# Optimization experiments

Measured on AMD Instinct MI355X. Metric: run time of the kernel, lower is better.

The kernel has to match this reference:

```python
import jax, jax.numpy as jnp
import numpy as np

N_NODES, IN_F, HIDDEN, N_EDGES, N_TRAIN, N_CLASS = 50000, 64, 512, 160000, 80000, 7
BN_EPS = 1e-5

def _lin(k, fin, fout):
    return jax.random.normal(k, (fin, fout), jnp.float32) * 0.05, jnp.zeros((fout,), jnp.float32)

def setup_inputs() -> dict:
    key = jax.random.key(0)
    ks = jax.random.split(key, 12)
    x = jax.random.normal(ks[0], (N_NODES, IN_F), jnp.float32)
    edge_index = jax.random.randint(ks[1], (2, N_EDGES), 0, N_NODES, jnp.int32)
    train_edge_id = jax.random.randint(ks[2], (N_TRAIN,), 0, N_EDGES, jnp.int32)
    W1, b1 = _lin(ks[3], IN_F, HIDDEN)
    W2, b2 = _lin(ks[4], HIDDEN, HIDDEN)
    W3, b3 = _lin(ks[5], HIDDEN, HIDDEN)
    W4, b4 = _lin(ks[6], HIDDEN, HIDDEN)
    lin1_W, lin1_b = _lin(ks[7], HIDDEN, HIDDEN)
    lin2_W, lin2_b = _lin(ks[8], HIDDEN, HIDDEN)
    fc2_W, fc2_b = _lin(ks[9], HIDDEN, N_CLASS)
    ones = jnp.ones((HIDDEN,), jnp.float32); zeros = jnp.zeros((HIDDEN,), jnp.float32)
    return dict(x=x, edge_index=edge_index, train_edge_id=train_edge_id,
                W1=W1, b1=b1, W2=W2, b2=b2, W3=W3, b3=b3,
                bn1_g=ones, bn1_b=zeros, bn1_m=zeros, bn1_v=ones, eps1=jnp.float32(0.0),
                W4=W4, b4=b4, bn2_g=ones, bn2_b=zeros, bn2_m=zeros, bn2_v=ones, eps2=jnp.float32(0.0),
                lin1_W=lin1_W, lin1_b=lin1_b, lin2_W=lin2_W, lin2_b=lin2_b,
                fc2_W=fc2_W, fc2_b=fc2_b)

def _gin_agg(h, src, dst, eps):
    # PyG GINConv: (1+eps)*x_i + sum_{j in N(i)} x_j, messages flow src->dst
    agg = jax.ops.segment_sum(h[src], dst, num_segments=N_NODES)
    return (1.0 + eps) * h + agg

def _bn(h, g, b, m, v):
    return (h - m) * jax.lax.rsqrt(v + BN_EPS) * g + b

def reference(x, edge_index, train_edge_id, W1, b1, W2, b2, W3, b3,
              bn1_g, bn1_b, bn1_m, bn1_v, eps1,
              W4, b4, bn2_g, bn2_b, bn2_m, bn2_v, eps2,
              lin1_W, lin1_b, lin2_W, lin2_b, fc2_W, fc2_b):
    src, dst = edge_index[0], edge_index[1]
    h = _gin_agg(x, src, dst, eps1)
    h = jax.nn.relu(h @ W1 + b1)
    h = jax.nn.relu(h @ W2 + b2)
    h = jax.nn.relu(h @ W3 + b3)
    h = _bn(h, bn1_g, bn1_b, bn1_m, bn1_v)
    # gin_convs[0]: agg -> Linear+ReLU -> BN
    h = _gin_agg(h, src, dst, eps2)
    h = jax.nn.relu(h @ W4 + b4)
    h = _bn(h, bn2_g, bn2_b, bn2_m, bn2_v)
    # node MLP head (dropout = identity in eval)
    h = jax.nn.relu(h @ lin1_W + lin1_b)
    h = h @ lin2_W + lin2_b
    # edge-gather fusion (feature_fusion=None -> elementwise mul)
    node_id = edge_index[:, train_edge_id]  # [2, T]
    x1 = h[node_id[0]]
    x2 = h[node_id[1]]
    return (x1 * x2) @ fc2_W + fc2_b  # [T, class_num]
```

## Files before the change

kernel.cpp:

```cpp
#include <hip/hip_runtime.h>

#define N_NODES 50000
#define MPAD    50048
#define IN_F    64
#define HIDDEN  512
#define N_EDGES 160000
#define N_TRAIN 80000
#define N_CLASS 7
#define BN_EPS  1e-5f

#define MT      (MPAD / 128)
#define NT      4
#define FULLGRP ((MT / 8) * 32)

typedef short  bf16x8 __attribute__((ext_vector_type(8)));
typedef float  f32x4  __attribute__((ext_vector_type(4)));
typedef unsigned short ushort_t;

__device__ __forceinline__ ushort_t f2b(float v) {
    union { float f; unsigned int u; } c; c.f = v;
    unsigned int x = c.u;
    unsigned int r = (x + 0x7FFFu + ((x >> 16) & 1u)) >> 16;
    return (ushort_t)r;
}
__device__ __forceinline__ float b2f(ushort_t b) {
    union { unsigned int u; float f; } c; c.u = ((unsigned int)b) << 16;
    return c.f;
}

__device__ __forceinline__ void async_copy16(const void* g, void* l) {
    __builtin_amdgcn_global_load_lds(
        (const __attribute__((address_space(1))) void*)g,
        (__attribute__((address_space(3))) void*)l, 16, 0, 0);
}

__global__ void zero_kernel(int* __restrict__ p, int n) {
    int i = blockIdx.x * blockDim.x + threadIdx.x;
    if (i < n) p[i] = 0;
}

__global__ void hist_kernel(const int* __restrict__ ei, int* __restrict__ deg) {
    int e = blockIdx.x * blockDim.x + threadIdx.x;
    if (e >= N_EDGES) return;
    atomicAdd(&deg[ei[N_EDGES + e]], 1);
}

__global__ __launch_bounds__(1024) void scan_kernel(const int* __restrict__ deg,
                                                    int* __restrict__ rowptr) {
    __shared__ int buf[1024];
    __shared__ int carry_s;
    int tid = threadIdx.x;
    if (tid == 0) { carry_s = 0; rowptr[0] = 0; }
    __syncthreads();
    for (int base = 0; base < N_NODES; base += 1024) {
        int i = base + tid;
        buf[tid] = (i < N_NODES) ? deg[i] : 0;
        __syncthreads();
        for (int off = 1; off < 1024; off <<= 1) {
            int t = (tid >= off) ? buf[tid - off] : 0;
            __syncthreads();
            buf[tid] += t;
            __syncthreads();
        }
        if (i < N_NODES) rowptr[i + 1] = buf[tid] + carry_s;
        __syncthreads();
        if (tid == 0) carry_s += buf[1023];
        __syncthreads();
    }
}

__global__ void cursor_init_kernel(const int* __restrict__ rowptr,
                                   int* __restrict__ cursor) {
    int i = blockIdx.x * blockDim.x + threadIdx.x;
    if (i < N_NODES) cursor[i] = rowptr[i];
}

__global__ void scatter_kernel(const int* __restrict__ ei,
                               int* __restrict__ cursor, int* __restrict__ adj) {
    int e = blockIdx.x * blockDim.x + threadIdx.x;
    if (e >= N_EDGES) return;
    int src = ei[e], dst = ei[N_EDGES + e];
    int pos = atomicAdd(&cursor[dst], 1);
    adj[pos] = src;
}

__global__ __launch_bounds__(256) void gather64_kernel(
    const float* __restrict__ x, const int* __restrict__ rowptr,
    const int* __restrict__ adj, const float* __restrict__ epsp,
    ushort_t* __restrict__ hi, ushort_t* __restrict__ lo) {
    int wave = threadIdx.x >> 6, lane = threadIdx.x & 63;
    int n = blockIdx.x * 4 + wave;
    if (n >= N_NODES) return;
    float s = 1.0f + *epsp;
    float sum = s * x[(size_t)n * IN_F + lane];
    int beg = rowptr[n], end = rowptr[n + 1];
    for (int k = beg; k < end; k++) {
        sum += x[(size_t)adj[k] * IN_F + lane];
    }
    ushort_t hb = f2b(sum);
    ushort_t lb = f2b(sum - b2f(hb));
    hi[(size_t)n * IN_F + lane] = hb;
    lo[(size_t)n * IN_F + lane] = lb;
}

__global__ __launch_bounds__(256) void gather512_kernel(
    const float* __restrict__ h, const int* __restrict__ rowptr,
    const int* __restrict__ adj, const float* __restrict__ epsp,
    ushort_t* __restrict__ hi, ushort_t* __restrict__ lo) {
    int wave = threadIdx.x >> 6, lane = threadIdx.x & 63;
    int n = blockIdx.x * 4 + wave;
    if (n >= N_NODES) return;
    float s = 1.0f + *epsp;
    const float* hn = h + (size_t)n * HIDDEN;
    const int f0 = lane * 4, f1 = 256 + lane * 4;
    float4 a0 = *(const float4*)&hn[f0];
    float4 a1 = *(const float4*)&hn[f1];
    float sum0[4] = {s * a0.x, s * a0.y, s * a0.z, s * a0.w};
    float sum1[4] = {s * a1.x, s * a1.y, s * a1.z, s * a1.w};
    int beg = rowptr[n], end = rowptr[n + 1];
    for (int k = beg; k < end; k++) {
        const float* hs = h + (size_t)adj[k] * HIDDEN;
        float4 b0 = *(const float4*)&hs[f0];
        float4 b1 = *(const float4*)&hs[f1];
        sum0[0] += b0.x; sum0[1] += b0.y; sum0[2] += b0.z; sum0[3] += b0.w;
        sum1[0] += b1.x; sum1[1] += b1.y; sum1[2] += b1.z; sum1[3] += b1.w;
    }
    ushort_t h4[4], l4[4];
#pragma unroll
    for (int j = 0; j < 4; j++) {
        h4[j] = f2b(sum0[j]);
        l4[j] = f2b(sum0[j] - b2f(h4[j]));
    }
    *(ushort4*)&hi[(size_t)n * HIDDEN + f0] = make_ushort4(h4[0], h4[1], h4[2], h4[3]);
    *(ushort4*)&lo[(size_t)n * HIDDEN + f0] = make_ushort4(l4[0], l4[1], l4[2], l4[3]);
#pragma unroll
    for (int j = 0; j < 4; j++) {
        h4[j] = f2b(sum1[j]);
        l4[j] = f2b(sum1[j] - b2f(h4[j]));
    }
    *(ushort4*)&hi[(size_t)n * HIDDEN + f1] = make_ushort4(h4[0], h4[1], h4[2], h4[3]);
    *(ushort4*)&lo[(size_t)n * HIDDEN + f1] = make_ushort4(l4[0], l4[1], l4[2], l4[3]);
}

__global__ void wtrans_kernel(const float* __restrict__ W,
                              ushort_t* __restrict__ Whi,
                              ushort_t* __restrict__ Wlo, int K) {
    __shared__ float t[32][33];
    int tx = threadIdx.x & 31, ty = threadIdx.x >> 5;
    int nb = blockIdx.x * 32, kb = blockIdx.y * 32;
#pragma unroll
    for (int i = 0; i < 4; i++) {
        int k = kb + ty + i * 8;
        t[ty + i * 8][tx] = W[(size_t)k * HIDDEN + nb + tx];
    }
    __syncthreads();
#pragma unroll
    for (int i = 0; i < 4; i++) {
        int n = nb + ty + i * 8;
        int k = kb + tx;
        float v = t[tx][ty + i * 8];
        ushort_t hb = f2b(v);
        ushort_t lb = f2b(v - b2f(hb));
        Whi[(size_t)n * K + k] = hb;
        Wlo[(size_t)n * K + k] = lb;
    }
}

__global__ __launch_bounds__(256) void gemm_split_kernel(
    const ushort_t* __restrict__ Ahi, const ushort_t* __restrict__ Alo,
    const ushort_t* __restrict__ Bhi, const ushort_t* __restrict__ Blo,
    const float* __restrict__ bias,
    float* __restrict__ Cf, ushort_t* __restrict__ Chi, ushort_t* __restrict__ Clo,
    int K, int mode,
    const float* __restrict__ bn_g, const float* __restrict__ bn_b,
    const float* __restrict__ bn_m, const float* __restrict__ bn_v) {
    __shared__ ushort_t As_h[128 * 32];
    __shared__ ushort_t As_l[128 * 32];
    __shared__ ushort_t Bs_h[128 * 32];
    __shared__ ushort_t Bs_l[128 * 32];

    const int tid  = threadIdx.x;
    const int wave = tid >> 6, lane = tid & 63;
    const int wm = wave >> 1, wn = wave & 1;
    const int quad = lane >> 4, r = lane & 15;

    int idx = blockIdx.x, m_t, n_t;
    if (idx < FULLGRP) {
        m_t = (idx >> 5) * 8 + (idx & 7);
        n_t = (idx >> 3) & 3;
    } else {
        int t = idx - FULLGRP;
        m_t = (FULLGRP >> 2) + (t >> 2);
        n_t = t & 3;
    }
    const int m0 = m_t * 128, n0 = n_t * 128;

    const f32x4 vzero = {0.f, 0.f, 0.f, 0.f};
    f32x4 acc[4][4];
#pragma unroll
    for (int i = 0; i < 4; i++)
#pragma unroll
        for (int j = 0; j < 4; j++) acc[i][j] = vzero;

    const int srow = (lane >> 2);
    const int scol = (lane & 3) * 8;

    for (int k0 = 0; k0 < K; k0 += 32) {
        __syncthreads();
#pragma unroll
        for (int t = 0; t < 2; t++) {
            int rr = wave * 32 + t * 16 + srow;
            int lbase = (wave * 32 + t * 16) * 32;
            size_t ga = (size_t)(m0 + rr) * K + k0 + scol;
            size_t gb = (size_t)(n0 + rr) * K + k0 + scol;
            async_copy16(Ahi + ga, &As_h[lbase]);
            async_copy16(Alo + ga, &As_l[lbase]);
            async_copy16(Bhi + gb, &Bs_h[lbase]);
            async_copy16(Blo + gb, &Bs_l[lbase]);
        }
        __syncthreads();

        bf16x8 ah[4], al[4], bh[4], bl[4];
#pragma unroll
        for (int i = 0; i < 4; i++) {
            int aofs = (wm * 64 + i * 16 + r) * 32 + quad * 8;
            int bofs = (wn * 64 + i * 16 + r) * 32 + quad * 8;
            ah[i] = *(const bf16x8*)&As_h[aofs];
            al[i] = *(const bf16x8*)&As_l[aofs];
            bh[i] = *(const bf16x8*)&Bs_h[bofs];
            bl[i] = *(const bf16x8*)&Bs_l[bofs];
        }
#pragma unroll
        for (int i = 0; i < 4; i++)
#pragma unroll
            for (int j = 0; j < 4; j++) {
                acc[i][j] = __builtin_amdgcn_mfma_f32_16x16x32_bf16(ah[i], bh[j], acc[i][j], 0, 0, 0);
                acc[i][j] = __builtin_amdgcn_mfma_f32_16x16x32_bf16(ah[i], bl[j], acc[i][j], 0, 0, 0);
                acc[i][j] = __builtin_amdgcn_mfma_f32_16x16x32_bf16(al[i], bh[j], acc[i][j], 0, 0, 0);
            }
    }

    float bia[4], sc[4], sh[4];
#pragma unroll
    for (int j = 0; j < 4; j++) {
        int col = n0 + wn * 64 + j * 16 + r;
        bia[j] = bias[col];
        if (mode == 2) {
            float g = bn_g[col], bb = bn_b[col], mm = bn_m[col], vv = bn_v[col];
            sc[j] = g * rsqrtf(vv + BN_EPS);
            sh[j] = bb - mm * sc[j];
        } else { sc[j] = 1.f; sh[j] = 0.f; }
    }
#pragma unroll
    for (int i = 0; i < 4; i++) {
#pragma unroll
        for (int rg = 0; rg < 4; rg++) {
            int row = m0 + wm * 64 + i * 16 + quad * 4 + rg;
            if (row >= N_NODES) continue;
#pragma unroll
            for (int j = 0; j < 4; j++) {
                int col = n0 + wn * 64 + j * 16 + r;
                float v = acc[i][j][rg] + bia[j];
                if (mode >= 1) v = fmaxf(v, 0.f);
                if (mode == 2) v = v * sc[j] + sh[j];
                size_t idx2 = (size_t)row * HIDDEN + col;
                if (Cf) {
                    Cf[idx2] = v;
                } else {
                    ushort_t hb = f2b(v);
                    ushort_t lb = f2b(v - b2f(hb));
                    Chi[idx2] = hb;
                    Clo[idx2] = lb;
                }
            }
        }
    }
}

__global__ __launch_bounds__(256) void fc2_kernel(
    const float* __restrict__ h, const int* __restrict__ ei,
    const int* __restrict__ teid, const float* __restrict__ W,
    const float* __restrict__ bias, float* __restrict__ out) {
    __shared__ float Ws[HIDDEN * N_CLASS];
    __shared__ float bs[N_CLASS];
    for (int i = threadIdx.x; i < HIDDEN * N_CLASS; i += blockDim.x) Ws[i] = W[i];
    if (threadIdx.x < N_CLASS) bs[threadIdx.x] = bias[threadIdx.x];
    __syncthreads();

    int wave = threadIdx.x >> 6;
    int lane = threadIdx.x & 63;
    int t = blockIdx.x * 4 + wave;
    if (t >= N_TRAIN) return;

    int e = teid[t];
    int a = ei[e];
    int b = ei[N_EDGES + e];
    const float* xa = h + (size_t)a * HIDDEN;
    const float* xb = h + (size_t)b * HIDDEN;

    float acc[N_CLASS];
#pragma unroll
    for (int c = 0; c < N_CLASS; c++) acc[c] = 0.f;

    int j0 = lane * 8;
    float4 a0 = *(const float4*)&xa[j0];
    float4 a1 = *(const float4*)&xa[j0 + 4];
    float4 b0 = *(const float4*)&xb[j0];
    float4 b1 = *(const float4*)&xb[j0 + 4];
    float p[8] = {a0.x * b0.x, a0.y * b0.y, a0.z * b0.z, a0.w * b0.w,
                  a1.x * b1.x, a1.y * b1.y, a1.z * b1.z, a1.w * b1.w};
#pragma unroll
    for (int jj = 0; jj < 8; jj++) {
        const float* wrow = &Ws[(j0 + jj) * N_CLASS];
#pragma unroll
        for (int c = 0; c < N_CLASS; c++) acc[c] = fmaf(p[jj], wrow[c], acc[c]);
    }
#pragma unroll
    for (int c = 0; c < N_CLASS; c++) {
        float v = acc[c];
        for (int off = 32; off > 0; off >>= 1) v += __shfl_down(v, off, 64);
        if (lane == 0) out[(size_t)t * N_CLASS + c] = v + bs[c];
    }
}

extern "C" void kernel_launch(void* const* d_in, const int* in_sizes, int n_in,
                              void* d_out, int out_size, void* d_ws, size_t ws_size,
                              hipStream_t stream) {
    const float* x      = (const float*)d_in[0];
    const int*   ei     = (const int*)d_in[1];
    const int*   teid   = (const int*)d_in[2];
    const float* W1     = (const float*)d_in[3];
    const float* b1     = (const float*)d_in[4];
    const float* W2     = (const float*)d_in[5];
    const float* b2     = (const float*)d_in[6];
    const float* W3     = (const float*)d_in[7];
    const float* b3     = (const float*)d_in[8];
    const float* bn1_g  = (const float*)d_in[9];
    const float* bn1_b  = (const float*)d_in[10];
    const float* bn1_m  = (const float*)d_in[11];
    const float* bn1_v  = (const float*)d_in[12];
    const float* eps1   = (const float*)d_in[13];
    const float* W4     = (const float*)d_in[14];
    const float* b4     = (const float*)d_in[15];
    const float* bn2_g  = (const float*)d_in[16];
    const float* bn2_b  = (const float*)d_in[17];
    const float* bn2_m  = (const float*)d_in[18];
    const float* bn2_v  = (const float*)d_in[19];
    const float* eps2   = (const float*)d_in[20];
    const float* lin1_W = (const float*)d_in[21];
    const float* lin1_b = (const float*)d_in[22];
    const float* lin2_W = (const float*)d_in[23];
    const float* lin2_b = (const float*)d_in[24];
    const float* fc2_W  = (const float*)d_in[25];
    const float* fc2_b  = (const float*)d_in[26];

    const size_t PLANE   = (size_t)MPAD * HIDDEN;
    const size_t PLANE64 = (size_t)MPAD * IN_F;

    ushort_t* R0h = (ushort_t*)d_ws;
    ushort_t* R0l = R0h + PLANE;
    ushort_t* R1h = R0l + PLANE;
    ushort_t* R1l = R1h + PLANE;

    const size_t WSMALL = (size_t)HIDDEN * IN_F;
    const size_t WBIG   = (size_t)HIDDEN * HIDDEN;
    ushort_t* Wp   = R1l + PLANE;
    ushort_t* Wt1h = Wp;            ushort_t* Wt1l = Wt1h + WSMALL;
    ushort_t* Wt2h = Wt1l + WSMALL; ushort_t* Wt2l = Wt2h + WBIG;
    ushort_t* Wt3h = Wt2l + WBIG;   ushort_t* Wt3l = Wt3h + WBIG;
    ushort_t* Wt4h = Wt3l + WBIG;   ushort_t* Wt4l = Wt4h + WBIG;
    ushort_t* Wt5h = Wt4l + WBIG;   ushort_t* Wt5l = Wt5h + WBIG;
    ushort_t* Wt6h = Wt5l + WBIG;   ushort_t* Wt6l = Wt6h + WBIG;

    int* deg    = (int*)(Wt6l + WBIG);
    int* rowptr = deg + N_NODES;
    int* adj    = rowptr + (N_NODES + 1);

    float* F32_R0 = (float*)R0h;
    ushort_t* H0h = R1h;
    ushort_t* H0l = R1h + PLANE64;

    zero_kernel<<<(N_NODES + 255) / 256, 256, 0, stream>>>(deg, N_NODES);
    hist_kernel<<<(N_EDGES + 255) / 256, 256, 0, stream>>>(ei, deg);
    scan_kernel<<<1, 1024, 0, stream>>>(deg, rowptr);
    cursor_init_kernel<<<(N_NODES + 255) / 256, 256, 0, stream>>>(rowptr, deg);
    scatter_kernel<<<(N_EDGES + 255) / 256, 256, 0, stream>>>(ei, deg, adj);

    dim3 wtgS(HIDDEN / 32, IN_F / 32);
    dim3 wtgB(HIDDEN / 32, HIDDEN / 32);
    wtrans_kernel<<<wtgS, 256, 0, stream>>>(W1, Wt1h, Wt1l, IN_F);
    wtrans_kernel<<<wtgB, 256, 0, stream>>>(W2, Wt2h, Wt2l, HIDDEN);
    wtrans_kernel<<<wtgB, 256, 0, stream>>>(W3, Wt3h, Wt3l, HIDDEN);
    wtrans_kernel<<<wtgB, 256, 0, stream>>>(W4, Wt4h, Wt4l, HIDDEN);
    wtrans_kernel<<<wtgB, 256, 0, stream>>>(lin1_W, Wt5h, Wt5l, HIDDEN);
    wtrans_kernel<<<wtgB, 256, 0, stream>>>(lin2_W, Wt6h, Wt6l, HIDDEN);

    const int ngrid = MT * NT;
    int nwb = (N_NODES + 3) / 4;

    gather64_kernel<<<nwb, 256, 0, stream>>>(x, rowptr, adj, eps1, H0h, H0l);

    gemm_split_kernel<<<ngrid, 256, 0, stream>>>(H0h, H0l, Wt1h, Wt1l, b1,
        nullptr, R0h, R0l, IN_F, 1, nullptr, nullptr, nullptr, nullptr);
    gemm_split_kernel<<<ngrid, 256, 0, stream>>>(R0h, R0l, Wt2h, Wt2l, b2,
        nullptr, R1h, R1l, HIDDEN, 1, nullptr, nullptr, nullptr, nullptr);
    gemm_split_kernel<<<ngrid, 256, 0, stream>>>(R1h, R1l, Wt3h, Wt3l, b3,
        F32_R0, nullptr, nullptr, HIDDEN, 2, bn1_g, bn1_b, bn1_m, bn1_v);

    gather512_kernel<<<nwb, 256, 0, stream>>>(F32_R0, rowptr, adj, eps2, R1h, R1l);

    gemm_split_kernel<<<ngrid, 256, 0, stream>>>(R1h, R1l, Wt4h, Wt4l, b4,
        nullptr, R0h, R0l, HIDDEN, 2, bn2_g, bn2_b, bn2_m, bn2_v);
    gemm_split_kernel<<<ngrid, 256, 0, stream>>>(R0h, R0l, Wt5h, Wt5l, lin1_b,
        nullptr, R1h, R1l, HIDDEN, 1, nullptr, nullptr, nullptr, nullptr);
    gemm_split_kernel<<<ngrid, 256, 0, stream>>>(R1h, R1l, Wt6h, Wt6l, lin2_b,
        F32_R0, nullptr, nullptr, HIDDEN, 0, nullptr, nullptr, nullptr, nullptr);

    fc2_kernel<<<(N_TRAIN + 3) / 4, 256, 0, stream>>>(F32_R0, ei, teid, fc2_W, fc2_b,
                                                      (float*)d_out);
}
```

Measured before the change: 1.046 ms.

## Load GEMM fragments directly from global memory, dropping LDS staging

The split-bf16 GEMM no longer stages A/B tiles through shared memory with async global-to-LDS copies and two barriers per k-step. Each wave instead loads its MFMA operand fragments straight from global memory, and K becomes a template parameter so the loop can be unrolled. This removes the barriers and the LDS round trip. In exchange there is no data reuse across waves in a block, so each tile is fetched twice from global/L2, and the 16-byte loads are strided per row.

```diff
diff --git a/kernel.cpp b/kernel.cpp
--- a/kernel.cpp
+++ b/kernel.cpp
@@ -26,12 +26,6 @@
 __device__ __forceinline__ float b2f(ushort_t b) {
     union { unsigned int u; float f; } c; c.u = ((unsigned int)b) << 16;
     return c.f;
-}
-
-__device__ __forceinline__ void async_copy16(const void* g, void* l) {
-    __builtin_amdgcn_global_load_lds(
-        (const __attribute__((address_space(1))) void*)g,
-        (__attribute__((address_space(3))) void*)l, 16, 0, 0);
 }
 
 __global__ void zero_kernel(int* __restrict__ p, int n) {
@@ -166,19 +160,15 @@
     }
 }
 
-__global__ __launch_bounds__(256) void gemm_split_kernel(
+template<int K>
+__global__ __launch_bounds__(256) void gemm_direct_kernel(
     const ushort_t* __restrict__ Ahi, const ushort_t* __restrict__ Alo,
     const ushort_t* __restrict__ Bhi, const ushort_t* __restrict__ Blo,
     const float* __restrict__ bias,
     float* __restrict__ Cf, ushort_t* __restrict__ Chi, ushort_t* __restrict__ Clo,
-    int K, int mode,
+    int mode,
     const float* __restrict__ bn_g, const float* __restrict__ bn_b,
     const float* __restrict__ bn_m, const float* __restrict__ bn_v) {
-    __shared__ ushort_t As_h[128 * 32];
-    __shared__ ushort_t As_l[128 * 32];
-    __shared__ ushort_t Bs_h[128 * 32];
-    __shared__ ushort_t Bs_l[128 * 32];
-
     const int tid  = threadIdx.x;
     const int wave = tid >> 6, lane = tid & 63;
     const int wm = wave >> 1, wn = wave & 1;
@@ -202,33 +192,23 @@
 #pragma unroll
         for (int j = 0; j < 4; j++) acc[i][j] = vzero;
 
-    const int srow = (lane >> 2);
-    const int scol = (lane & 3) * 8;
-
+    const size_t aoff = (size_t)(m0 + wm * 64 + r) * K + quad * 8;
+    const size_t boff = (size_t)(n0 + wn * 64 + r) * K + quad * 8;
+    const ushort_t* Ah = Ahi + aoff;
+    const ushort_t* Al = Alo + aoff;
+    const ushort_t* Bh = Bhi + boff;
+    const ushort_t* Bl = Blo + boff;
+    const size_t rstep = (size_t)16 * K;
+
+#pragma unroll 2
     for (int k0 = 0; k0 < K; k0 += 32) {
-        __syncthreads();
-#pragma unroll
-        for (int t = 0; t < 2; t++) {
-            int rr = wave * 32 + t * 16 + srow;
-            int lbase = (wave * 32 + t * 16) * 32;
-            size_t ga = (size_t)(m0 + rr) * K + k0 + scol;
-            size_t gb = (size_t)(n0 + rr) * K + k0 + scol;
-            async_copy16(Ahi + ga, &As_h[lbase]);
-            async_copy16(Alo + ga, &As_l[lbase]);
-            async_copy16(Bhi + gb, &Bs_h[lbase]);
-            async_copy16(Blo + gb, &Bs_l[lbase]);
-        }
-        __syncthreads();
-
         bf16x8 ah[4], al[4], bh[4], bl[4];
 #pragma unroll
         for (int i = 0; i < 4; i++) {
-            int aofs = (wm * 64 + i * 16 + r) * 32 + quad * 8;
-            int bofs = (wn * 64 + i * 16 + r) * 32 + quad * 8;
-            ah[i] = *(const bf16x8*)&As_h[aofs];
-            al[i] = *(const bf16x8*)&As_l[aofs];
-            bh[i] = *(const bf16x8*)&Bs_h[bofs];
-            bl[i] = *(const bf16x8*)&Bs_l[bofs];
+            ah[i] = *(const bf16x8*)(Ah + i * rstep + k0);
+            al[i] = *(const bf16x8*)(Al + i * rstep + k0);
+            bh[i] = *(const bf16x8*)(Bh + i * rstep + k0);
+            bl[i] = *(const bf16x8*)(Bl + i * rstep + k0);
         }
 #pragma unroll
         for (int i = 0; i < 4; i++)
@@ -263,14 +243,14 @@
                 float v = acc[i][j][rg] + bia[j];
                 if (mode >= 1) v = fmaxf(v, 0.f);
                 if (mode == 2) v = v * sc[j] + sh[j];
-                size_t idx2 = (size_t)row * HIDDEN + col;
+                size_t oix = (size_t)row * HIDDEN + col;
                 if (Cf) {
-                    Cf[idx2] = v;
+                    Cf[oix] = v;
                 } else {
                     ushort_t hb = f2b(v);
                     ushort_t lb = f2b(v - b2f(hb));
-                    Chi[idx2] = hb;
-                    Clo[idx2] = lb;
+                    Chi[oix] = hb;
+                    Clo[oix] = lb;
                 }
             }
         }
@@ -400,21 +380,21 @@
 
     gather64_kernel<<<nwb, 256, 0, stream>>>(x, rowptr, adj, eps1, H0h, H0l);
 
-    gemm_split_kernel<<<ngrid, 256, 0, stream>>>(H0h, H0l, Wt1h, Wt1l, b1,
-        nullptr, R0h, R0l, IN_F, 1, nullptr, nullptr, nullptr, nullptr);
-    gemm_split_kernel<<<ngrid, 256, 0, stream>>>(R0h, R0l, Wt2h, Wt2l, b2,
-        nullptr, R1h, R1l, HIDDEN, 1, nullptr, nullptr, nullptr, nullptr);
-    gemm_split_kernel<<<ngrid, 256, 0, stream>>>(R1h, R1l, Wt3h, Wt3l, b3,
-        F32_R0, nullptr, nullptr, HIDDEN, 2, bn1_g, bn1_b, bn1_m, bn1_v);
+    gemm_direct_kernel<IN_F><<<ngrid, 256, 0, stream>>>(H0h, H0l, Wt1h, Wt1l, b1,
+        nullptr, R0h, R0l, 1, nullptr, nullptr, nullptr, nullptr);
+    gemm_direct_kernel<HIDDEN><<<ngrid, 256, 0, stream>>>(R0h, R0l, Wt2h, Wt2l, b2,
+        nullptr, R1h, R1l, 1, nullptr, nullptr, nullptr, nullptr);
+    gemm_direct_kernel<HIDDEN><<<ngrid, 256, 0, stream>>>(R1h, R1l, Wt3h, Wt3l, b3,
+        F32_R0, nullptr, nullptr, 2, bn1_g, bn1_b, bn1_m, bn1_v);
 
     gather512_kernel<<<nwb, 256, 0, stream>>>(F32_R0, rowptr, adj, eps2, R1h, R1l);
 
-    gemm_split_kernel<<<ngrid, 256, 0, stream>>>(R1h, R1l, Wt4h, Wt4l, b4,
-        nullptr, R0h, R0l, HIDDEN, 2, bn2_g, bn2_b, bn2_m, bn2_v);
-    gemm_split_kernel<<<ngrid, 256, 0, stream>>>(R0h, R0l, Wt5h, Wt5l, lin1_b,
-        nullptr, R1h, R1l, HIDDEN, 1, nullptr, nullptr, nullptr, nullptr);
-    gemm_split_kernel<<<ngrid, 256, 0, stream>>>(R1h, R1l, Wt6h, Wt6l, lin2_b,
-        F32_R0, nullptr, nullptr, HIDDEN, 0, nullptr, nullptr, nullptr, nullptr);
+    gemm_direct_kernel<HIDDEN><<<ngrid, 256, 0, stream>>>(R1h, R1l, Wt4h, Wt4l, b4,
+        nullptr, R0h, R0l, 2, bn2_g, bn2_b, bn2_m, bn2_v);
+    gemm_direct_kernel<HIDDEN><<<ngrid, 256, 0, stream>>>(R0h, R0l, Wt5h, Wt5l, lin1_b,
+        nullptr, R1h, R1l, 1, nullptr, nullptr, nullptr, nullptr);
+    gemm_direct_kernel<HIDDEN><<<ngrid, 256, 0, stream>>>(R1h, R1l, Wt6h, Wt6l, lin2_b,
+        F32_R0, nullptr, nullptr, 0, nullptr, nullptr, nullptr, nullptr);
 
     fc2_kernel<<<(N_TRAIN + 3) / 4, 256, 0, stream>>>(F32_R0, ei, teid, fc2_W, fc2_b,
                                                       (float*)d_out);
```

New measurement: 1.639 ms. 1.57x slower.
